# Kernel optimization log

Measured on AMD Instinct MI355X. Metric: run time of the kernel, lower is better.

Reference implementation:

```python
import jax, jax.numpy as jnp
import numpy as np

EMBED_DIM = 512
NUM_HEADS = 8
HEAD_DIM = EMBED_DIM // NUM_HEADS


def setup_inputs() -> dict:
    key = jax.random.key(0)
    ks = jax.random.split(key, 5)
    B, N, D = 2, 4096, EMBED_DIM
    s_in = 1.0 / np.sqrt(D)
    x = jax.random.normal(ks[0], (B, N, D), dtype=jnp.float32)
    qkv_w = jax.random.uniform(ks[1], (3 * D, D), dtype=jnp.float32, minval=-s_in, maxval=s_in)
    qkv_b = jax.random.uniform(ks[2], (3 * D,), dtype=jnp.float32, minval=-s_in, maxval=s_in)
    out_w = jax.random.uniform(ks[3], (D, D), dtype=jnp.float32, minval=-s_in, maxval=s_in)
    out_b = jax.random.uniform(ks[4], (D,), dtype=jnp.float32, minval=-s_in, maxval=s_in)
    return {"x": x, "qkv_w": qkv_w, "qkv_b": qkv_b, "out_w": out_w, "out_b": out_b}


def reference(x, qkv_w, qkv_b, out_w, out_b):
    B, N, D = x.shape
    H, Hd = NUM_HEADS, HEAD_DIM
    # qkv projection: [B,N,3D] -> [3,B,H,N,Hd]
    qkv = x @ qkv_w.T + qkv_b
    qkv = qkv.reshape(B, N, 3, H, Hd).transpose(2, 0, 3, 1, 4)
    q, k, v = qkv[0], qkv[1], qkv[2]
    scale = 1.0 / jnp.sqrt(jnp.asarray(Hd, dtype=x.dtype))
    scores = jnp.einsum("bhnd,bhmd->bhnm", q, k) * scale  # [B,H,N,N]
    weights = jax.nn.softmax(scores, axis=-1)
    out = jnp.einsum("bhnm,bhmd->bhnd", weights, v)  # [B,H,N,Hd]
    out = out.transpose(0, 2, 1, 3).reshape(B, N, D)
    return out @ out_w.T + out_b
```

## Files before the change

### kernel.cpp

```cpp
#include <hip/hip_runtime.h>

typedef __attribute__((ext_vector_type(8))) short short8;
typedef __attribute__((ext_vector_type(2))) float f32x2;
typedef __attribute__((ext_vector_type(4))) float f32x4;
typedef __attribute__((ext_vector_type(16))) float f32x16;
typedef unsigned short u16;
typedef unsigned int u32;

#define SCQ 0.18033688011112042f

__device__ __forceinline__ u16 f2b(float f) {
  unsigned u = __builtin_bit_cast(unsigned, f);
  u += 0x7FFFu + ((u >> 16) & 1u);
  return (u16)(u >> 16);
}

__device__ __forceinline__ u32 cvtpk(float a, float b) {
  u32 r;
  asm("v_cvt_pk_bf16_f32 %0, %1, %2" : "=v"(r) : "v"(a), "v"(b));
  return r;
}

__device__ __forceinline__ float ex2(float x) { return __builtin_amdgcn_exp2f(x); }

__device__ __forceinline__ void gl_lds16(const u16* g, u16* l) {
  __builtin_amdgcn_global_load_lds(
      (const __attribute__((address_space(1))) unsigned int*)g,
      (__attribute__((address_space(3))) unsigned int*)l, 16, 0, 0);
}

__global__ __launch_bounds__(256) void convert_k(
    const float* __restrict__ x, const float* __restrict__ w1, const float* __restrict__ w2,
    u16* __restrict__ xb, u16* __restrict__ w1b, u16* __restrict__ w2b) {
  const int NXv = (8192 * 512) / 4;
  const int NW1v = (1536 * 512) / 4;
  const int NW2v = (512 * 512) / 4;
  int i = blockIdx.x * 256 + threadIdx.x;
  const float4* src;
  u16* dst;
  int j;
  float scale = 1.0f;
  if (i < NXv) {
    src = (const float4*)x; dst = xb; j = i;
  } else if (i < NXv + NW1v) {
    j = i - NXv; src = (const float4*)w1; dst = w1b;
    if (j < (512 * 512) / 4) scale = SCQ;
  } else {
    j = i - NXv - NW1v;
    if (j >= NW2v) return;
    src = (const float4*)w2; dst = w2b;
  }
  float4 v = src[j];
  ushort4 o;
  o.x = f2b(v.x * scale); o.y = f2b(v.y * scale);
  o.z = f2b(v.z * scale); o.w = f2b(v.w * scale);
  *reinterpret_cast<ushort4*>(dst + (size_t)j * 4) = o;
}

__global__ __launch_bounds__(256) void qkv_gemm(
    const u16* __restrict__ Ab, const u16* __restrict__ Bw, const float* __restrict__ bias,
    u16* __restrict__ Qd, u16* __restrict__ Kd, u16* __restrict__ Vtd) {
  const int m0 = blockIdx.x * 128, n0 = blockIdx.y * 128;
  const int tid = threadIdx.x, wave = tid >> 6, lane = tid & 63;
  const int g = lane >> 4, lr = lane & 15;
  const int wm = (wave >> 1) * 64, wn = (wave & 1) * 64;
  __shared__ alignas(16) u16 smem[32768];

  f32x4 acc[4][4];
#pragma unroll
  for (int mf = 0; mf < 4; ++mf)
#pragma unroll
    for (int nf = 0; nf < 4; ++nf)
#pragma unroll
      for (int r = 0; r < 4; ++r) acc[mf][nf][r] = 0.0f;

  const int gid0 = wave * 64 + lane;

#define QKV_STAGE(buf, k0)                                                         \
  {                                                                                \
    u16* Ad_ = smem + (buf) * 8192;                                                \
    u16* Bd_ = smem + 16384 + (buf) * 8192;                                        \
    _Pragma("unroll")                                                              \
    for (int c = 0; c < 4; ++c) {                                                  \
      const int gid = c * 256 + gid0;                                              \
      const int row = gid >> 3;                                                    \
      const int col = ((gid & 7) ^ (row & 7)) << 3;                                \
      gl_lds16(Ab + (size_t)(m0 + row) * 512 + (k0) + col,                         \
               Ad_ + (size_t)(c * 256 + wave * 64) * 8);                           \
      gl_lds16(Bw + (size_t)(n0 + row) * 512 + (k0) + col,                         \
               Bd_ + (size_t)(c * 256 + wave * 64) * 8);                           \
    }                                                                              \
  }

  QKV_STAGE(0, 0);
  __syncthreads();

#pragma unroll 1
  for (int kt = 0; kt < 8; ++kt) {
    const int cur = kt & 1;
    if (kt + 1 < 8) QKV_STAGE(cur ^ 1, (kt + 1) * 64);

    const u16* Ac = smem + cur * 8192;
    const u16* Bc = smem + 16384 + cur * 8192;
#pragma unroll
    for (int kb = 0; kb < 2; ++kb) {
      short8 bf[4], af[4];
#pragma unroll
      for (int nf = 0; nf < 4; ++nf)
        bf[nf] = *reinterpret_cast<const short8*>(
            &Bc[(wn + nf * 16 + lr) * 64 + (((kb * 4 + g) ^ (lr & 7)) << 3)]);
#pragma unroll
      for (int mf = 0; mf < 4; ++mf)
        af[mf] = *reinterpret_cast<const short8*>(
            &Ac[(wm + mf * 16 + lr) * 64 + (((kb * 4 + g) ^ (lr & 7)) << 3)]);
#pragma unroll
      for (int mf = 0; mf < 4; ++mf)
#pragma unroll
        for (int nf = 0; nf < 4; ++nf)
          acc[mf][nf] = __builtin_amdgcn_mfma_f32_16x16x32_bf16(af[mf], bf[nf], acc[mf][nf], 0, 0, 0);
    }
    __syncthreads();
  }
#undef QKV_STAGE

  u16* Ct = smem;
  const int b = m0 >> 12;
  const int which = n0 >> 9;
  const int nloc = m0 & 4095;

  if (which < 2) {
#pragma unroll
    for (int mf = 0; mf < 4; ++mf)
#pragma unroll
      for (int nf = 0; nf < 4; ++nf) {
        const int col_l = wn + nf * 16 + lr;
        float bv = bias[n0 + col_l];
        if (which == 0) bv *= SCQ;
#pragma unroll
        for (int r = 0; r < 4; ++r)
          Ct[(wm + mf * 16 + g * 4 + r) * 136 + col_l] = f2b(acc[mf][nf][r] + bv);
      }
    __syncthreads();
    u16* const dst0 = (which == 0) ? Qd : Kd;
#pragma unroll
    for (int p = 0; p < 8; ++p) {
      const int idx = p * 256 + tid;
      const int row = idx >> 4;
      const int c8 = (idx & 15) << 3;
      short8 v = *reinterpret_cast<const short8*>(&Ct[row * 136 + c8]);
      const int col = n0 + c8;
      const int h = (col & 511) >> 6, hd = col & 63;
      *reinterpret_cast<short8*>(
          dst0 + ((size_t)(b * 8 + h) * 4096 + nloc + row) * 64 + hd) = v;
    }
  } else {
#pragma unroll
    for (int mf = 0; mf < 4; ++mf)
#pragma unroll
      for (int nf = 0; nf < 4; ++nf) {
        const int col_l = wn + nf * 16 + lr;
        const float bv = bias[n0 + col_l];
        const int row0 = wm + mf * 16 + g * 4;
        ushort4 pk;
        pk.x = f2b(acc[mf][nf][0] + bv);
        pk.y = f2b(acc[mf][nf][1] + bv);
        pk.z = f2b(acc[mf][nf][2] + bv);
        pk.w = f2b(acc[mf][nf][3] + bv);
        *reinterpret_cast<ushort4*>(&Ct[col_l * 136 + row0]) = pk;
      }
    __syncthreads();
#pragma unroll
    for (int p = 0; p < 8; ++p) {
      const int idx = p * 256 + tid;
      const int col_l = idx >> 4;
      const int c8 = (idx & 15) << 3;
      short8 v = *reinterpret_cast<const short8*>(&Ct[col_l * 136 + c8]);
      const int col = n0 + col_l;
      const int h = (col & 511) >> 6, hd = col & 63;
      *reinterpret_cast<short8*>(
          Vtd + ((size_t)(b * 8 + h) * 64 + hd) * 4096 + nloc + c8) = v;
    }
  }
}

__global__ __launch_bounds__(256, 2) void attn13(
    const u16* __restrict__ Qd, const u16* __restrict__ Kd, const u16* __restrict__ Vtd,
    float* __restrict__ Op, float* __restrict__ Lp) {
  int f = blockIdx.x;
  int xcd = f & 7, slot = f >> 3;
  int bh = (xcd << 1) + (slot >> 5);
  int rem = slot & 31;
  int half = rem >> 4;
  int qb = rem & 15;

  const int tid = threadIdx.x, wave = tid >> 6, lane = tid & 63;
  const int hi = lane >> 5, lq = lane & 31;

  const u16* Qh = Qd + (size_t)bh * (4096 * 64);
  const u16* Kh = Kd + (size_t)bh * (4096 * 64);
  const u16* Vh = Vtd + (size_t)bh * (64 * 4096);
  float* Oh = Op + (size_t)half * (8192 * 512);
  float* Lh = Lp + (size_t)half * (16 * 4096);

  __shared__ alignas(16) u16 Kl[2][128 * 64];

  const int qrow_base = qb * 256 + wave * 64;

  short8 qf[2][4];
#pragma unroll
  for (int qt = 0; qt < 2; ++qt)
#pragma unroll
    for (int s = 0; s < 4; ++s)
      qf[qt][s] = *reinterpret_cast<const short8*>(
          Qh + (size_t)(qrow_base + qt * 32 + lq) * 64 + s * 16 + hi * 8);

  f32x16 acc[2][2];
#pragma unroll
  for (int qt = 0; qt < 2; ++qt)
#pragma unroll
    for (int dt = 0; dt < 2; ++dt)
#pragma unroll
      for (int i = 0; i < 16; ++i) acc[qt][dt][i] = 0.0f;

  f32x16 Z;
#pragma unroll
  for (int i = 0; i < 16; ++i) Z[i] = 0.0f;

  float lrun[2] = {0.0f, 0.0f};

  const int kv0 = half * 2048;
  const int gid0 = wave * 64 + lane;

#pragma unroll
  for (int c = 0; c < 4; ++c) {
    const int gid = c * 256 + gid0;
    const int row = gid >> 3;
    const int col = ((gid & 7) ^ (row & 7)) << 3;
    gl_lds16(Kh + (size_t)(kv0 + row) * 64 + col, &Kl[0][(c * 256 + wave * 64) * 8]);
  }
  __syncthreads();

  f32x16 stA0, stA1, stB0, stB1;
  short8 vfA[2][2], vfB[2][2];
  short8 pbA0[2], pbA1[2], pbB0[2], pbB1[2];

#define QK_HALF(st0, st1, h)                                                        \
  {                                                                                 \
    const int rb = ((h) * 32 + lq) * 64;                                            \
    __builtin_amdgcn_s_setprio(1);                                                  \
    _Pragma("unroll")                                                               \
    for (int s = 0; s < 4; ++s) {                                                   \
      const int ch = ((2 * s + hi) ^ (lq & 7)) << 3;                                \
      short8 kf = *reinterpret_cast<const short8*>(&Kl[cur][rb + ch]);              \
      if (s == 0) {                                                                 \
        st0 = __builtin_amdgcn_mfma_f32_32x32x16_bf16(kf, qf[0][0], Z, 0, 0, 0);    \
        st1 = __builtin_amdgcn_mfma_f32_32x32x16_bf16(kf, qf[1][0], Z, 0, 0, 0);    \
      } else {                                                                      \
        st0 = __builtin_amdgcn_mfma_f32_32x32x16_bf16(kf, qf[0][s], st0, 0, 0, 0);  \
        st1 = __builtin_amdgcn_mfma_f32_32x32x16_bf16(kf, qf[1][s], st1, 0, 0, 0);  \
      }                                                                             \
    }                                                                               \
    __builtin_amdgcn_s_setprio(0);                                                  \
  }

#define LOADV_HALF(vf, h)                                                           \
  {                                                                                 \
    const int off = kbase + (h) * 32 + hi * 8;                                      \
    vf[0][0] = *reinterpret_cast<const short8*>(Vh + (size_t)lq * 4096 + off);      \
    vf[0][1] = *reinterpret_cast<const short8*>(Vh + (size_t)(32 + lq) * 4096 + off); \
    vf[1][0] = *reinterpret_cast<const short8*>(Vh + (size_t)lq * 4096 + off + 16); \
    vf[1][1] = *reinterpret_cast<const short8*>(Vh + (size_t)(32 + lq) * 4096 + off + 16); \
  }

#define SM_QT(stq, pbq, qt_idx)                                                     \
  {                                                                                 \
    f32x2 p2[8];                                                                    \
    _Pragma("unroll")                                                               \
    for (int j = 0; j < 8; ++j) {                                                   \
      p2[j][0] = ex2(stq[2 * j]);                                                   \
      p2[j][1] = ex2(stq[2 * j + 1]);                                               \
    }                                                                               \
    f32x2 s0 = (p2[0] + p2[1]) + (p2[2] + p2[3]);                                   \
    f32x2 s1 = (p2[4] + p2[5]) + (p2[6] + p2[7]);                                   \
    f32x2 sm = s0 + s1;                                                             \
    lrun[qt_idx] += sm[0] + sm[1];                                                  \
    _Pragma("unroll")                                                               \
    for (int t = 0; t < 2; ++t) {                                                   \
      u32 wa = cvtpk(p2[4 * t + 0][0], p2[4 * t + 0][1]);                           \
      u32 wb = cvtpk(p2[4 * t + 2][0], p2[4 * t + 2][1]);                           \
      u32 wc = cvtpk(p2[4 * t + 1][0], p2[4 * t + 1][1]);                           \
      u32 wd = cvtpk(p2[4 * t + 3][0], p2[4 * t + 3][1]);                           \
      asm volatile("v_permlane32_swap_b32 %0, %1" : "+v"(wa), "+v"(wb));            \
      asm volatile("v_permlane32_swap_b32 %0, %1" : "+v"(wc), "+v"(wd));            \
      int4 wv;                                                                      \
      wv.x = (int)wa; wv.y = (int)wc; wv.z = (int)wb; wv.w = (int)wd;               \
      pbq[t] = __builtin_bit_cast(short8, wv);                                      \
    }                                                                               \
  }

#define PV_HALF(vf, pb0, pb1)                                                       \
  {                                                                                 \
    __builtin_amdgcn_s_setprio(1);                                                  \
    _Pragma("unroll")                                                               \
    for (int t = 0; t < 2; ++t) {                                                   \
      acc[0][0] = __builtin_amdgcn_mfma_f32_32x32x16_bf16(vf[t][0], pb0[t], acc[0][0], 0, 0, 0); \
      acc[0][1] = __builtin_amdgcn_mfma_f32_32x32x16_bf16(vf[t][1], pb0[t], acc[0][1], 0, 0, 0); \
      acc[1][0] = __builtin_amdgcn_mfma_f32_32x32x16_bf16(vf[t][0], pb1[t], acc[1][0], 0, 0, 0); \
      acc[1][1] = __builtin_amdgcn_mfma_f32_32x32x16_bf16(vf[t][1], pb1[t], acc[1][1], 0, 0, 0); \
    }                                                                               \
    __builtin_amdgcn_s_setprio(0);                                                  \
  }

#pragma unroll 1
  for (int kt = 0; kt < 16; ++kt) {
    const int cur = kt & 1;
    const int kbase = kv0 + kt * 128;

    if (kt + 1 < 16) {
      const u16* kn = Kh + (size_t)(kbase + 128) * 64;
#pragma unroll
      for (int c = 0; c < 4; ++c) {
        const int gid = c * 256 + gid0;
        const int row = gid >> 3;
        const int col = ((gid & 7) ^ (row & 7)) << 3;
        gl_lds16(kn + (size_t)row * 64 + col, &Kl[cur ^ 1][(c * 256 + wave * 64) * 8]);
      }
    }

    QK_HALF(stA0, stA1, 0);
    LOADV_HALF(vfA, 0);
#pragma unroll
    for (int hp = 0; hp < 2; ++hp) {
      const int h = hp * 2;
      QK_HALF(stB0, stB1, h + 1);
      LOADV_HALF(vfB, h + 1);
      SM_QT(stA0, pbA0, 0);
      SM_QT(stA1, pbA1, 1);
      PV_HALF(vfA, pbA0, pbA1);
      if (hp == 0) {
        QK_HALF(stA0, stA1, h + 2);
        LOADV_HALF(vfA, h + 2);
      }
      SM_QT(stB0, pbB0, 0);
      SM_QT(stB1, pbB1, 1);
      PV_HALF(vfB, pbB0, pbB1);
    }

    __syncthreads();
  }
#undef QK_HALF
#undef LOADV_HALF
#undef SM_QT
#undef PV_HALF

  const int b = bh >> 3, h = bh & 7;
#pragma unroll
  for (int qt = 0; qt < 2; ++qt) {
    const int qn = qrow_base + qt * 32 + lq;
    const size_t rowoff = ((size_t)(b * 4096 + qn)) * 512 + h * 64;
#pragma unroll
    for (int dt = 0; dt < 2; ++dt)
#pragma unroll
      for (int t = 0; t < 4; ++t) {
        f32x4 v4;
        v4[0] = acc[qt][dt][4 * t + 0];
        v4[1] = acc[qt][dt][4 * t + 1];
        v4[2] = acc[qt][dt][4 * t + 2];
        v4[3] = acc[qt][dt][4 * t + 3];
        *reinterpret_cast<f32x4*>(Oh + rowoff + dt * 32 + t * 8 + hi * 4) = v4;
      }
    float lt = lrun[qt] + __shfl_xor(lrun[qt], 32);
    if (hi == 0) Lh[(bh << 12) + qn] = lt;
  }
}

__global__ __launch_bounds__(256) void combine_k(
    const float* __restrict__ Op, const float* __restrict__ Lp,
    u16* __restrict__ attnb) {
  int idx = blockIdx.x * 256 + threadIdx.x;
  int row = idx >> 7, c4 = idx & 127;
  int b = row >> 12, n = row & 4095, h = c4 >> 4;
  int li = (((b << 3) + h) << 12) + n;
  float l = Lp[li] + Lp[li + 65536];
  float inv = 1.0f / l;
  const int STRIDE = 8192 * 512 / 4;
  float4 o0 = reinterpret_cast<const float4*>(Op)[idx];
  float4 o1 = reinterpret_cast<const float4*>(Op)[idx + STRIDE];
  ushort4 o;
  o.x = f2b((o0.x + o1.x) * inv);
  o.y = f2b((o0.y + o1.y) * inv);
  o.z = f2b((o0.z + o1.z) * inv);
  o.w = f2b((o0.w + o1.w) * inv);
  *reinterpret_cast<ushort4*>(attnb + (size_t)idx * 4) = o;
}

__global__ __launch_bounds__(256) void out_gemm(
    const u16* __restrict__ Ab, const u16* __restrict__ Bw, const float* __restrict__ bias,
    float* __restrict__ out) {
  const int m0 = blockIdx.x * 128, n0 = blockIdx.y * 64;
  const int tid = threadIdx.x, wave = tid >> 6, lane = tid & 63;
  const int g = lane >> 4, lr = lane & 15;
  const int wm = (wave >> 1) * 64, wn = (wave & 1) * 32;
  __shared__ alignas(16) u16 Al[128][72];
  __shared__ alignas(16) u16 Bl[64][72];

  f32x4 acc[4][2];
#pragma unroll
  for (int mf = 0; mf < 4; ++mf)
#pragma unroll
    for (int nf = 0; nf < 2; ++nf)
#pragma unroll
      for (int r = 0; r < 4; ++r) acc[mf][nf][r] = 0.0f;

  const int rr = tid >> 3, cc = tid & 7;
  for (int k0 = 0; k0 < 512; k0 += 64) {
    __syncthreads();
#pragma unroll
    for (int it = 0; it < 4; ++it)
      *reinterpret_cast<short8*>(&Al[rr + it * 32][cc * 8]) =
          *reinterpret_cast<const short8*>(Ab + (size_t)(m0 + rr + it * 32) * 512 + k0 + cc * 8);
#pragma unroll
    for (int it = 0; it < 2; ++it)
      *reinterpret_cast<short8*>(&Bl[rr + it * 32][cc * 8]) =
          *reinterpret_cast<const short8*>(Bw + (size_t)(n0 + rr + it * 32) * 512 + k0 + cc * 8);
    __syncthreads();
#pragma unroll
    for (int kb = 0; kb < 2; ++kb) {
      short8 bf[2], af[4];
#pragma unroll
      for (int nf = 0; nf < 2; ++nf)
        bf[nf] = *reinterpret_cast<const short8*>(&Bl[wn + nf * 16 + lr][kb * 32 + g * 8]);
#pragma unroll
      for (int mf = 0; mf < 4; ++mf)
        af[mf] = *reinterpret_cast<const short8*>(&Al[wm + mf * 16 + lr][kb * 32 + g * 8]);
#pragma unroll
      for (int mf = 0; mf < 4; ++mf)
#pragma unroll
        for (int nf = 0; nf < 2; ++nf)
          acc[mf][nf] = __builtin_amdgcn_mfma_f32_16x16x32_bf16(af[mf], bf[nf], acc[mf][nf], 0, 0, 0);
    }
  }
#pragma unroll
  for (int mf = 0; mf < 4; ++mf)
#pragma unroll
    for (int nf = 0; nf < 2; ++nf)
#pragma unroll
      for (int r = 0; r < 4; ++r) {
        int row = m0 + wm + mf * 16 + g * 4 + r;
        int col = n0 + wn + nf * 16 + lr;
        out[(size_t)row * 512 + col] = acc[mf][nf][r] + bias[col];
      }
}

extern "C" void kernel_launch(void* const* d_in, const int* in_sizes, int n_in,
                              void* d_out, int out_size, void* d_ws, size_t ws_size,
                              hipStream_t stream) {
  const float* x = (const float*)d_in[0];
  const float* qkv_w = (const float*)d_in[1];
  const float* qkv_b = (const float*)d_in[2];
  const float* out_w = (const float*)d_in[3];
  const float* out_b = (const float*)d_in[4];
  float* out = (float*)d_out;

  char* ws = (char*)d_ws;
  u16* xb    = (u16*)(ws + 0);
  u16* w1b   = (u16*)(ws + 8388608);
  u16* w2b   = (u16*)(ws + 9961472);
  u16* Qd    = (u16*)(ws + 10485760);
  u16* Kd    = (u16*)(ws + 18874368);
  u16* Vtd   = (u16*)(ws + 27262976);
  u16* attnb = (u16*)(ws + 35651584);
  float* Op  = (float*)(ws + 44040192);
  float* Lp  = (float*)(ws + 77594624);

  convert_k<<<5120, 256, 0, stream>>>(x, qkv_w, out_w, xb, w1b, w2b);
  qkv_gemm<<<dim3(64, 12), 256, 0, stream>>>(xb, w1b, qkv_b, Qd, Kd, Vtd);
  attn13<<<512, 256, 0, stream>>>(Qd, Kd, Vtd, Op, Lp);
  combine_k<<<4096, 256, 0, stream>>>(Op, Lp, attnb);
  out_gemm<<<dim3(64, 8), 256, 0, stream>>>(attnb, w2b, out_b, out);
}
```

Baseline: 131.6 us.

## Double-buffer out_gemm with direct global-to-LDS loads, swizzle, and 128x128 tiles

Rewrites the output projection GEMM to use 128x128 block tiles, so each block does twice the work and half as many blocks launch. Tiles are staged into LDS through a global-to-LDS copy helper (presumably defined in the unseen part of the file) with an XOR swizzle, and the loads are double-buffered so the next K tile is fetched while the current one is multiplied. This aims to hide global load latency and reduce LDS bank conflicts. In exchange it uses more LDS and accumulator registers per block and launches fewer blocks (256).

```diff
diff --git a/kernel.cpp b/kernel.cpp
--- a/kernel.cpp
+++ b/kernel.cpp
@@ -397,53 +397,73 @@
 __global__ __launch_bounds__(256) void out_gemm(
     const u16* __restrict__ Ab, const u16* __restrict__ Bw, const float* __restrict__ bias,
     float* __restrict__ out) {
-  const int m0 = blockIdx.x * 128, n0 = blockIdx.y * 64;
+  const int m0 = blockIdx.x * 128, n0 = blockIdx.y * 128;
   const int tid = threadIdx.x, wave = tid >> 6, lane = tid & 63;
   const int g = lane >> 4, lr = lane & 15;
-  const int wm = (wave >> 1) * 64, wn = (wave & 1) * 32;
-  __shared__ alignas(16) u16 Al[128][72];
-  __shared__ alignas(16) u16 Bl[64][72];
-
-  f32x4 acc[4][2];
+  const int wm = (wave >> 1) * 64, wn = (wave & 1) * 64;
+  __shared__ alignas(16) u16 smem[32768];
+
+  f32x4 acc[4][4];
 #pragma unroll
   for (int mf = 0; mf < 4; ++mf)
 #pragma unroll
-    for (int nf = 0; nf < 2; ++nf)
+    for (int nf = 0; nf < 4; ++nf)
 #pragma unroll
       for (int r = 0; r < 4; ++r) acc[mf][nf][r] = 0.0f;
 
-  const int rr = tid >> 3, cc = tid & 7;
-  for (int k0 = 0; k0 < 512; k0 += 64) {
-    __syncthreads();
-#pragma unroll
-    for (int it = 0; it < 4; ++it)
-      *reinterpret_cast<short8*>(&Al[rr + it * 32][cc * 8]) =
-          *reinterpret_cast<const short8*>(Ab + (size_t)(m0 + rr + it * 32) * 512 + k0 + cc * 8);
-#pragma unroll
-    for (int it = 0; it < 2; ++it)
-      *reinterpret_cast<short8*>(&Bl[rr + it * 32][cc * 8]) =
-          *reinterpret_cast<const short8*>(Bw + (size_t)(n0 + rr + it * 32) * 512 + k0 + cc * 8);
-    __syncthreads();
+  const int gid0 = wave * 64 + lane;
+
+#define OUT_STAGE(buf, k0)                                                         \
+  {                                                                                \
+    u16* Ad_ = smem + (buf) * 8192;                                                \
+    u16* Bd_ = smem + 16384 + (buf) * 8192;                                        \
+    _Pragma("unroll")                                                              \
+    for (int c = 0; c < 4; ++c) {                                                  \
+      const int gid = c * 256 + gid0;                                              \
+      const int row = gid >> 3;                                                    \
+      const int col = ((gid & 7) ^ (row & 7)) << 3;                                \
+      gl_lds16(Ab + (size_t)(m0 + row) * 512 + (k0) + col,                         \
+               Ad_ + (size_t)(c * 256 + wave * 64) * 8);                           \
+      gl_lds16(Bw + (size_t)(n0 + row) * 512 + (k0) + col,                         \
+               Bd_ + (size_t)(c * 256 + wave * 64) * 8);                           \
+    }                                                                              \
+  }
+
+  OUT_STAGE(0, 0);
+  __syncthreads();
+
+#pragma unroll 1
+  for (int kt = 0; kt < 8; ++kt) {
+    const int cur = kt & 1;
+    if (kt + 1 < 8) OUT_STAGE(cur ^ 1, (kt + 1) * 64);
+
+    const u16* Ac = smem + cur * 8192;
+    const u16* Bc = smem + 16384 + cur * 8192;
 #pragma unroll
     for (int kb = 0; kb < 2; ++kb) {
-      short8 bf[2], af[4];
-#pragma unroll
-      for (int nf = 0; nf < 2; ++nf)
-        bf[nf] = *reinterpret_cast<const short8*>(&Bl[wn + nf * 16 + lr][kb * 32 + g * 8]);
+      short8 bf[4], af[4];
+#pragma unroll
+      for (int nf = 0; nf < 4; ++nf)
+        bf[nf] = *reinterpret_cast<const short8*>(
+            &Bc[(wn + nf * 16 + lr) * 64 + (((kb * 4 + g) ^ (lr & 7)) << 3)]);
 #pragma unroll
       for (int mf = 0; mf < 4; ++mf)
-        af[mf] = *reinterpret_cast<const short8*>(&Al[wm + mf * 16 + lr][kb * 32 + g * 8]);
+        af[mf] = *reinterpret_cast<const short8*>(
+            &Ac[(wm + mf * 16 + lr) * 64 + (((kb * 4 + g) ^ (lr & 7)) << 3)]);
 #pragma unroll
       for (int mf = 0; mf < 4; ++mf)
 #pragma unroll
-        for (int nf = 0; nf < 2; ++nf)
+        for (int nf = 0; nf < 4; ++nf)
           acc[mf][nf] = __builtin_amdgcn_mfma_f32_16x16x32_bf16(af[mf], bf[nf], acc[mf][nf], 0, 0, 0);
     }
-  }
+    __syncthreads();
+  }
+#undef OUT_STAGE
+
 #pragma unroll
   for (int mf = 0; mf < 4; ++mf)
 #pragma unroll
-    for (int nf = 0; nf < 2; ++nf)
+    for (int nf = 0; nf < 4; ++nf)
 #pragma unroll
       for (int r = 0; r < 4; ++r) {
         int row = m0 + wm + mf * 16 + g * 4 + r;
@@ -477,5 +497,5 @@
   qkv_gemm<<<dim3(64, 12), 256, 0, stream>>>(xb, w1b, qkv_b, Qd, Kd, Vtd);
   attn13<<<512, 256, 0, stream>>>(Qd, Kd, Vtd, Op, Lp);
   combine_k<<<4096, 256, 0, stream>>>(Op, Lp, attnb);
-  out_gemm<<<dim3(64, 8), 256, 0, stream>>>(attnb, w2b, out_b, out);
-}
+  out_gemm<<<dim3(64, 4), 256, 0, stream>>>(attnb, w2b, out_b, out);
+}
```

After: 131.4 us, median of 2. No clear change (-0.1%).
